# Kernel optimization log

Hardware: AMD Instinct MI355X
Metric: run time of the kernel (lower is better)

## Reference

```python
import jax, jax.numpy as jnp
import numpy as np

EPS = 1e-06
N_HEADS = 32
HEAD_DIM = 128
D_STATE = 128
D_MODEL = 2048
D_INNER = 4096
BATCH = 64


def setup_inputs() -> dict:
    key = jax.random.key(0)
    ks = jax.random.split(key, 8)
    bc_dim = N_HEADS * D_STATE
    theta_dim = N_HEADS * (D_STATE // 2)
    proj_dim = 2 * D_INNER + 2 * bc_dim + 2 * N_HEADS + theta_dim  # 18496
    x = jax.random.normal(ks[0], (BATCH, D_MODEL), jnp.float32)
    h = jax.random.normal(ks[1], (BATCH, N_HEADS, D_STATE, HEAD_DIM), jnp.float32) * 0.1
    B_prev = jax.random.normal(ks[2], (BATCH, N_HEADS, D_STATE), jnp.float32)
    x_prev = jax.random.normal(ks[3], (BATCH, N_HEADS, HEAD_DIM), jnp.float32)
    theta_cumsum = jax.random.normal(ks[4], (BATCH, N_HEADS, D_STATE // 2), jnp.float32)
    W_in = jax.random.normal(ks[5], (proj_dim, D_MODEL), jnp.float32) * 0.02
    # A_log initialized as log(arange(1, d_state+1)) repeated per head
    A_log = jnp.log(jnp.arange(1, D_STATE + 1, dtype=jnp.float32))[None, :].repeat(N_HEADS, axis=0)
    B_bias = jnp.ones((N_HEADS, D_STATE), jnp.float32)
    C_bias = jnp.ones((N_HEADS, D_STATE), jnp.float32)
    W_out = jax.random.normal(ks[6], (D_MODEL, D_INNER), jnp.float32) * 0.02
    return {"x": x, "h": h, "B_prev": B_prev, "x_prev": x_prev,
            "theta_cumsum": theta_cumsum, "W_in": W_in, "A_log": A_log,
            "B_bias": B_bias, "C_bias": C_bias, "W_out": W_out}


def _rms_norm(v):
    # RMS over last dim (v already fp32)
    rms = jnp.sqrt(jnp.mean(v * v, axis=-1, keepdims=True) + EPS)
    return v / rms


def _apply_rope(v, freqs):
    # v: (B,H,N), freqs: (B,H,N//2); interleaved pairs
    vp = v.reshape(*v.shape[:-1], -1, 2)
    c, s = jnp.cos(freqs), jnp.sin(freqs)
    v0, v1 = vp[..., 0], vp[..., 1]
    y0 = v0 * c - v1 * s
    y1 = v0 * s + v1 * c
    return jnp.stack([y0, y1], axis=-1).reshape(v.shape)


def reference(x, h, B_prev, x_prev, theta_cumsum, W_in, A_log, B_bias, C_bias, W_out):
    batch = x.shape[0]
    bc_dim = N_HEADS * D_STATE
    proj = x @ W_in.T  # (B, proj_dim)
    idx = 0
    x_proj = proj[:, idx:idx + D_INNER]; idx += D_INNER
    z = proj[:, idx:idx + D_INNER]; idx += D_INNER
    B_raw = proj[:, idx:idx + bc_dim]; idx += bc_dim
    C_raw = proj[:, idx:idx + bc_dim]; idx += bc_dim
    dt_raw = proj[:, idx:idx + N_HEADS]; idx += N_HEADS
    lam_raw = proj[:, idx:idx + N_HEADS]; idx += N_HEADS
    theta = proj[:, idx:].reshape(batch, N_HEADS, D_STATE // 2)

    x_proj = x_proj.reshape(batch, N_HEADS, HEAD_DIM)
    z = z.reshape(batch, N_HEADS, HEAD_DIM)
    B_raw = B_raw.reshape(batch, N_HEADS, D_STATE)
    C_raw = C_raw.reshape(batch, N_HEADS, D_STATE)

    B = _rms_norm(B_raw) + B_bias
    C = _rms_norm(C_raw) + C_bias

    dt = jax.nn.softplus(dt_raw)                       # (B,H)
    theta_cumsum_new = theta_cumsum + theta * dt[:, :, None]
    B = _apply_rope(B, theta_cumsum_new)
    C = _apply_rope(C, theta_cumsum_new)

    lam = jax.nn.sigmoid(lam_raw)                      # (B,H)
    A = -jnp.mean(jnp.exp(A_log), axis=-1)             # (H,)
    alpha = jnp.exp(dt * A)                            # (B,H)
    beta = (1.0 - lam) * dt * alpha
    gamma = lam * dt

    Bx_prev = jnp.einsum('bhn,bhp->bhnp', B_prev, x_prev)
    Bx_curr = jnp.einsum('bhn,bhp->bhnp', B, x_proj)
    h_new = (alpha[:, :, None, None] * h
             + beta[:, :, None, None] * Bx_prev
             + gamma[:, :, None, None] * Bx_curr)      # (B,H,N,P)

    y = jnp.einsum('bhn,bhnp->bhp', C, h_new)
    y = y * jax.nn.silu(z)
    y = y.reshape(batch, D_INNER) @ W_out.T            # (B, d_model)
    return y, h_new, B, x_proj, theta_cumsum_new
```

## Files before the change

kernel.cpp:

```cpp
#include <hip/hip_runtime.h>
#include <hip/hip_bf16.h>
#include <cstdint>
#include <cmath>

#define EPSV 1e-6f
#define PSTR 1183744

typedef __attribute__((ext_vector_type(8))) short bf16x8;
typedef __attribute__((ext_vector_type(4))) float f32x4;

typedef __attribute__((address_space(3))) unsigned int lds_u32;
typedef const __attribute__((address_space(1))) unsigned int g_u32;

__device__ __forceinline__ void load_lds16(const void* g, void* l) {
  __builtin_amdgcn_global_load_lds((g_u32*)g, (lds_u32*)l, 16, 0, 0);
}

__device__ __forceinline__ short f2b(float f) {
  unsigned u = __float_as_uint(f);
  u = (u + 0x7fffu + ((u >> 16) & 1u)) >> 16;
  return (short)u;
}

__device__ __forceinline__ bf16x8 cvt8(float4 a, float4 b) {
  bf16x8 v;
  v[0]=f2b(a.x); v[1]=f2b(a.y); v[2]=f2b(a.z); v[3]=f2b(a.w);
  v[4]=f2b(b.x); v[5]=f2b(b.y); v[6]=f2b(b.z); v[7]=f2b(b.w);
  return v;
}

__global__ __launch_bounds__(256) void conv_bf16(
    const float* __restrict__ in, short* __restrict__ out, int n8) {
  const int i = blockIdx.x * 256 + threadIdx.x;
  if (i < n8) {
    float4 a = ((const float4*)in)[2 * i];
    float4 b = ((const float4*)in)[2 * i + 1];
    ((bf16x8*)out)[i] = cvt8(a, b);
  }
}

template<int KSPLIT, int NT>
__global__ __launch_bounds__(256, 2) void gemm_wlds(
    const short* __restrict__ Abf, const float* __restrict__ W,
    float* __restrict__ Outp, int N, int K) {
  __shared__ float Wlds[3][64 * 64];
  __shared__ short Alds[3][64 * 64];
  const int tid = threadIdx.x;
  const int lane = tid & 63;
  const int wv = tid >> 6;
  const int lrow = lane & 15, lk = lane >> 4;
  const int bid = blockIdx.x;
  const int ks = bid % KSPLIT;
  const int nblk = (bid / KSPLIT) * 64;
  const int kbase = ks * (NT * 64);

  f32x4 acc[4];
#pragma unroll
  for (int i = 0; i < 4; ++i) acc[i] = (f32x4){0.f, 0.f, 0.f, 0.f};

  auto stage = [&](int buf, int k0) {
#pragma unroll
    for (int j = 0; j < 4; ++j) {
      const int c = wv * 4 + j;
      const int r = c * 4 + (lane >> 4);
      const int g = (lane & 15) ^ (r & 15);
      load_lds16(W + (size_t)(nblk + r) * K + k0 + g * 4,
                 (char*)&Wlds[buf][0] + c * 1024);
    }
#pragma unroll
    for (int j = 0; j < 2; ++j) {
      const int c = wv * 2 + j;
      const int r = c * 8 + (lane >> 3);
      const int g = (lane & 7) ^ (r & 7);
      load_lds16(Abf + (size_t)r * K + k0 + g * 8,
                 (char*)&Alds[buf][0] + c * 1024);
    }
  };

  auto compute = [&](int buf) {
    const int wr = wv * 16 + lrow;
#pragma unroll
    for (int kc = 0; kc < 2; ++kc) {
      const int g0 = kc * 8 + lk * 2;
      const float4 wlo = *(const float4*)((const char*)&Wlds[buf][0]
                          + wr * 256 + ((g0 ^ (lrow & 15)) * 16));
      const float4 whi = *(const float4*)((const char*)&Wlds[buf][0]
                          + wr * 256 + (((g0 + 1) ^ (lrow & 15)) * 16));
      const bf16x8 wb = cvt8(wlo, whi);
#pragma unroll
      for (int mf = 0; mf < 4; ++mf) {
        const int ar = mf * 16 + lrow;
        const int ga = ((kc << 2) | lk) ^ (ar & 7);
        const bf16x8 av = *(const bf16x8*)((const char*)&Alds[buf][0]
                           + ar * 128 + ga * 16);
        acc[mf] = __builtin_amdgcn_mfma_f32_16x16x32_bf16(av, wb, acc[mf], 0, 0, 0);
      }
    }
  };

  stage(0, kbase);
  stage(1, kbase + 64);

  for (int t = 0; t < NT; ++t) {
    if (t < NT - 1) asm volatile("s_waitcnt vmcnt(6)");
    else            asm volatile("s_waitcnt vmcnt(0)");
    __builtin_amdgcn_sched_barrier(0);
    __builtin_amdgcn_s_barrier();
    __builtin_amdgcn_sched_barrier(0);
    compute(t % 3);
    if (t + 2 <= NT - 1) stage((t + 2) % 3, kbase + (t + 2) * 64);
  }

  float* ob = Outp + (size_t)ks * 64 * N + nblk + wv * 16 + lrow;
#pragma unroll
  for (int mf = 0; mf < 4; ++mf)
#pragma unroll
    for (int i = 0; i < 4; ++i)
      ob[(size_t)(mf * 16 + lk * 4 + i) * N] = acc[mf][i];
}

__device__ __forceinline__ float block_reduce_sum256(float v, float* red, int t) {
#pragma unroll
  for (int o = 32; o > 0; o >>= 1) v += __shfl_xor(v, o, 64);
  __syncthreads();
  if ((t & 63) == 0) red[t >> 6] = v;
  __syncthreads();
  return red[0] + red[1] + red[2] + red[3];
}

__global__ __launch_bounds__(256) void state_update(
    const float* __restrict__ pp, const float* __restrict__ h,
    const float* __restrict__ B_prev, const float* __restrict__ x_prev,
    const float* __restrict__ theta_cumsum, const float* __restrict__ A_log,
    const float* __restrict__ B_bias, const float* __restrict__ C_bias,
    float* __restrict__ o_h, float* __restrict__ o_B,
    float* __restrict__ o_xp, float* __restrict__ o_th,
    short* __restrict__ ysbf) {
  const int bid = blockIdx.x;
  const int b = bid >> 5, hd = bid & 31;
  const int t = threadIdx.x;
  const size_t pb = (size_t)b * 18496;
#define PJ(o) (pp[pb + (o)] + pp[PSTR + pb + (o)] + pp[2 * PSTR + pb + (o)] \
             + pp[3 * PSTR + pb + (o)])

  __shared__ float sB[128], sC[128], sBp[128], sXp[128], sXv[128];
  __shared__ float red[8];
  __shared__ float yred[8][128];

  float aval = (t < 128) ? expf(A_log[hd * 128 + t]) : 0.f;
  float brv  = (t < 128) ? PJ(8192 + hd * 128 + t) : 0.f;
  float crv  = (t < 128) ? PJ(12288 + hd * 128 + t) : 0.f;
  if (t < 128) {
    sBp[t] = B_prev[(size_t)bid * 128 + t];
    float xp = PJ(hd * 128 + t);
    sXp[t] = xp;
    o_xp[(size_t)bid * 128 + t] = xp;
    sXv[t] = x_prev[(size_t)bid * 128 + t];
  }
  float sumA  = block_reduce_sum256(aval, red, t);
  float sumB2 = block_reduce_sum256(brv * brv, red, t);
  float sumC2 = block_reduce_sum256(crv * crv, red, t);

  const float dt_raw  = PJ(16384 + hd);
  const float lam_raw = PJ(16416 + hd);
  const float dt  = (dt_raw > 20.f) ? dt_raw : log1pf(expf(dt_raw));
  const float lam = 1.f / (1.f + expf(-lam_raw));
  const float A     = -sumA * (1.f / 128.f);
  const float alpha = expf(dt * A);
  const float beta  = (1.f - lam) * dt * alpha;
  const float gamma = lam * dt;
  const float rb = rsqrtf(sumB2 * (1.f / 128.f) + EPSV);
  const float rc = rsqrtf(sumC2 * (1.f / 128.f) + EPSV);

  if (t < 64) {
    float b0 = PJ(8192 + hd * 128 + 2 * t);
    float b1 = PJ(8192 + hd * 128 + 2 * t + 1);
    float c0 = PJ(12288 + hd * 128 + 2 * t);
    float c1 = PJ(12288 + hd * 128 + 2 * t + 1);
    b0 = b0 * rb + B_bias[hd * 128 + 2 * t];
    b1 = b1 * rb + B_bias[hd * 128 + 2 * t + 1];
    c0 = c0 * rc + C_bias[hd * 128 + 2 * t];
    c1 = c1 * rc + C_bias[hd * 128 + 2 * t + 1];
    const float th = theta_cumsum[(size_t)bid * 64 + t]
                   + PJ(16448 + hd * 64 + t) * dt;
    o_th[(size_t)bid * 64 + t] = th;
    const float cth = cosf(th), sth = sinf(th);
    const float nb0 = b0 * cth - b1 * sth, nb1 = b0 * sth + b1 * cth;
    const float nc0 = c0 * cth - c1 * sth, nc1 = c0 * sth + c1 * cth;
    sB[2 * t] = nb0; sB[2 * t + 1] = nb1;
    sC[2 * t] = nc0; sC[2 * t + 1] = nc1;
    o_B[(size_t)bid * 128 + 2 * t] = nb0;
    o_B[(size_t)bid * 128 + 2 * t + 1] = nb1;
  }
  __syncthreads();

  const int p4 = t & 31, nb = t >> 5;
  const float4 xp4 = *(const float4*)&sXp[p4 * 4];
  const float4 xv4 = *(const float4*)&sXv[p4 * 4];
  const size_t hbase = (size_t)bid * 16384;
  float4 ya = {0.f, 0.f, 0.f, 0.f};
  for (int n = nb; n < 128; n += 8) {
    const float4 hv = *(const float4*)&h[hbase + n * 128 + p4 * 4];
    const float cb = gamma * sB[n];
    const float cp = beta * sBp[n];
    float4 hn;
    hn.x = alpha * hv.x + cp * xv4.x + cb * xp4.x;
    hn.y = alpha * hv.y + cp * xv4.y + cb * xp4.y;
    hn.z = alpha * hv.z + cp * xv4.z + cb * xp4.z;
    hn.w = alpha * hv.w + cp * xv4.w + cb * xp4.w;
    *(float4*)&o_h[hbase + n * 128 + p4 * 4] = hn;
    const float cn = sC[n];
    ya.x += cn * hn.x; ya.y += cn * hn.y; ya.z += cn * hn.z; ya.w += cn * hn.w;
  }
  *(float4*)&yred[nb][p4 * 4] = ya;
  __syncthreads();
  if (t < 128) {
    float y = 0.f;
#pragma unroll
    for (int j = 0; j < 8; ++j) y += yred[j][t];
    const float zv = PJ(4096 + hd * 128 + t);
    const float sig = 1.f / (1.f + expf(-zv));
    ysbf[(size_t)b * 4096 + hd * 128 + t] = f2b(y * zv * sig);
  }
#undef PJ
}

__global__ __launch_bounds__(256) void reduce_y(
    const float* __restrict__ yp, float* __restrict__ y, int n4) {
  const int i = blockIdx.x * 256 + threadIdx.x;
  if (i < n4) {
    float4 s = ((const float4*)yp)[i];
#pragma unroll
    for (int k = 1; k < 16; ++k) {
      float4 t = ((const float4*)(yp + (size_t)k * 131072))[i];
      s.x += t.x; s.y += t.y; s.z += t.z; s.w += t.w;
    }
    ((float4*)y)[i] = s;
  }
}

extern "C" void kernel_launch(void* const* d_in, const int* in_sizes, int n_in,
                              void* d_out, int out_size, void* d_ws, size_t ws_size,
                              hipStream_t stream) {
  const float* x            = (const float*)d_in[0];
  const float* h            = (const float*)d_in[1];
  const float* B_prev       = (const float*)d_in[2];
  const float* x_prev       = (const float*)d_in[3];
  const float* theta_cumsum = (const float*)d_in[4];
  const float* W_in         = (const float*)d_in[5];
  const float* A_log        = (const float*)d_in[6];
  const float* B_bias       = (const float*)d_in[7];
  const float* C_bias       = (const float*)d_in[8];
  const float* W_out        = (const float*)d_in[9];

  float* out  = (float*)d_out;
  float* o_y  = out;
  float* o_h  = out + 131072;
  float* o_B  = o_h + 33554432;
  float* o_xp = o_B + 262144;
  float* o_th = o_xp + 262144;

  float* pp   = (float*)d_ws;
  float* yp   = pp;
  short* xbf  = (short*)(pp + 4 * PSTR);
  short* ysbf = xbf + 131072;

  conv_bf16<<<dim3(64), dim3(256), 0, stream>>>(x, xbf, 16384);
  gemm_wlds<4, 8><<<dim3(289 * 4), dim3(256), 0, stream>>>(
      xbf, W_in, pp, 18496, 2048);
  state_update<<<dim3(2048), dim3(256), 0, stream>>>(
      pp, h, B_prev, x_prev, theta_cumsum, A_log, B_bias, C_bias,
      o_h, o_B, o_xp, o_th, ysbf);
  gemm_wlds<16, 4><<<dim3(32 * 16), dim3(256), 0, stream>>>(
      ysbf, W_out, yp, 2048, 4096);
  reduce_y<<<dim3(128), dim3(256), 0, stream>>>(yp, o_y, 32768);
}
```

Before: 118.2 us.

## Give each wave private LDS tiles and drop block barriers in GEMM

```diff
diff --git a/kernel.cpp b/kernel.cpp
--- a/kernel.cpp
+++ b/kernel.cpp
@@ -40,19 +40,19 @@
 }
 
 template<int KSPLIT, int NT>
-__global__ __launch_bounds__(256, 2) void gemm_wlds(
+__global__ __launch_bounds__(256, 2) void gemm_wave(
     const short* __restrict__ Abf, const float* __restrict__ W,
     float* __restrict__ Outp, int N, int K) {
-  __shared__ float Wlds[3][64 * 64];
-  __shared__ short Alds[3][64 * 64];
-  const int tid = threadIdx.x;
-  const int lane = tid & 63;
-  const int wv = tid >> 6;
+  __shared__ float Wl[4][3][16 * 32];
+  __shared__ short Al[4][3][64 * 32];
+  const int lane = threadIdx.x & 63;
+  const int wv = threadIdx.x >> 6;
   const int lrow = lane & 15, lk = lane >> 4;
   const int bid = blockIdx.x;
   const int ks = bid % KSPLIT;
   const int nblk = (bid / KSPLIT) * 64;
-  const int kbase = ks * (NT * 64);
+  const int n0 = nblk + wv * 16;
+  const int kbase = ks * (NT * 32);
 
   f32x4 acc[4];
 #pragma unroll
@@ -60,58 +60,50 @@
 
   auto stage = [&](int buf, int k0) {
 #pragma unroll
+    for (int j = 0; j < 2; ++j) {
+      const int r = j * 8 + (lane >> 3);
+      const int g = (lane & 7) ^ (r & 7);
+      load_lds16(W + (size_t)(n0 + r) * K + k0 + g * 4,
+                 (char*)&Wl[wv][buf][0] + j * 1024);
+    }
+#pragma unroll
     for (int j = 0; j < 4; ++j) {
-      const int c = wv * 4 + j;
-      const int r = c * 4 + (lane >> 4);
-      const int g = (lane & 15) ^ (r & 15);
-      load_lds16(W + (size_t)(nblk + r) * K + k0 + g * 4,
-                 (char*)&Wlds[buf][0] + c * 1024);
-    }
-#pragma unroll
-    for (int j = 0; j < 2; ++j) {
-      const int c = wv * 2 + j;
-      const int r = c * 8 + (lane >> 3);
-      const int g = (lane & 7) ^ (r & 7);
+      const int r = j * 16 + (lane >> 2);
+      const int g = (lane & 3) ^ ((r >> 1) & 3);
       load_lds16(Abf + (size_t)r * K + k0 + g * 8,
-                 (char*)&Alds[buf][0] + c * 1024);
+                 (char*)&Al[wv][buf][0] + j * 1024);
     }
   };
 
   auto compute = [&](int buf) {
-    const int wr = wv * 16 + lrow;
-#pragma unroll
-    for (int kc = 0; kc < 2; ++kc) {
-      const int g0 = kc * 8 + lk * 2;
-      const float4 wlo = *(const float4*)((const char*)&Wlds[buf][0]
-                          + wr * 256 + ((g0 ^ (lrow & 15)) * 16));
-      const float4 whi = *(const float4*)((const char*)&Wlds[buf][0]
-                          + wr * 256 + (((g0 + 1) ^ (lrow & 15)) * 16));
-      const bf16x8 wb = cvt8(wlo, whi);
-#pragma unroll
-      for (int mf = 0; mf < 4; ++mf) {
-        const int ar = mf * 16 + lrow;
-        const int ga = ((kc << 2) | lk) ^ (ar & 7);
-        const bf16x8 av = *(const bf16x8*)((const char*)&Alds[buf][0]
-                           + ar * 128 + ga * 16);
-        acc[mf] = __builtin_amdgcn_mfma_f32_16x16x32_bf16(av, wb, acc[mf], 0, 0, 0);
-      }
+    const float4 wlo = *(const float4*)((const char*)&Wl[wv][buf][0]
+                        + lrow * 128 + (((2 * lk)     ^ (lrow & 7)) * 16));
+    const float4 whi = *(const float4*)((const char*)&Wl[wv][buf][0]
+                        + lrow * 128 + (((2 * lk + 1) ^ (lrow & 7)) * 16));
+    const bf16x8 wb = cvt8(wlo, whi);
+#pragma unroll
+    for (int mf = 0; mf < 4; ++mf) {
+      const int ar = mf * 16 + lrow;
+      const int ga = lk ^ ((ar >> 1) & 3);
+      const bf16x8 av = *(const bf16x8*)((const char*)&Al[wv][buf][0]
+                         + ar * 64 + ga * 16);
+      acc[mf] = __builtin_amdgcn_mfma_f32_16x16x32_bf16(av, wb, acc[mf], 0, 0, 0);
     }
   };
 
   stage(0, kbase);
-  stage(1, kbase + 64);
+  stage(1, kbase + 32);
 
   for (int t = 0; t < NT; ++t) {
     if (t < NT - 1) asm volatile("s_waitcnt vmcnt(6)");
     else            asm volatile("s_waitcnt vmcnt(0)");
     __builtin_amdgcn_sched_barrier(0);
-    __builtin_amdgcn_s_barrier();
+    if (t + 2 <= NT - 1) stage((t + 2) % 3, kbase + (t + 2) * 32);
     __builtin_amdgcn_sched_barrier(0);
     compute(t % 3);
-    if (t + 2 <= NT - 1) stage((t + 2) % 3, kbase + (t + 2) * 64);
-  }
-
-  float* ob = Outp + (size_t)ks * 64 * N + nblk + wv * 16 + lrow;
+  }
+
+  float* ob = Outp + (size_t)ks * 64 * N + n0 + lrow;
 #pragma unroll
   for (int mf = 0; mf < 4; ++mf)
 #pragma unroll
@@ -266,12 +258,12 @@
   short* ysbf = xbf + 131072;
 
   conv_bf16<<<dim3(64), dim3(256), 0, stream>>>(x, xbf, 16384);
-  gemm_wlds<4, 8><<<dim3(289 * 4), dim3(256), 0, stream>>>(
+  gemm_wave<4, 16><<<dim3(289 * 4), dim3(256), 0, stream>>>(
       xbf, W_in, pp, 18496, 2048);
   state_update<<<dim3(2048), dim3(256), 0, stream>>>(
       pp, h, B_prev, x_prev, theta_cumsum, A_log, B_bias, C_bias,
       o_h, o_B, o_xp, o_th, ysbf);
-  gemm_wlds<16, 4><<<dim3(32 * 16), dim3(256), 0, stream>>>(
+  gemm_wave<16, 8><<<dim3(32 * 16), dim3(256), 0, stream>>>(
       ysbf, W_out, yp, 2048, 4096);
   reduce_y<<<dim3(128), dim3(256), 0, stream>>>(yp, o_y, 32768);
 }
```

After: 128.0 us. +8.2%, slower.

## Use 128-wide N tiles with 32-deep K steps for input projection GEMM

Applied to the files above, without the earlier changes.

```diff
diff --git a/kernel.cpp b/kernel.cpp
--- a/kernel.cpp
+++ b/kernel.cpp
@@ -40,14 +40,98 @@
 }
 
 template<int KSPLIT, int NT>
+__global__ __launch_bounds__(256, 2) void gemm_t128(
+    const short* __restrict__ Abf, const float* __restrict__ W,
+    float* __restrict__ Outp, int N, int K) {
+  __shared__ float Wlds[3][128 * 32];
+  __shared__ short Alds[3][64 * 32];
+  const int lane = threadIdx.x & 63;
+  const int wv = threadIdx.x >> 6;
+  const int lrow = lane & 15, lk = lane >> 4;
+  const int bid = blockIdx.x;
+  const int ks = bid % KSPLIT;
+  const int n0 = (bid / KSPLIT) * 128;
+  const int kbase = ks * (NT * 32);
+
+  f32x4 acc[2][4];
+#pragma unroll
+  for (int a = 0; a < 2; ++a)
+#pragma unroll
+    for (int b = 0; b < 4; ++b) acc[a][b] = (f32x4){0.f, 0.f, 0.f, 0.f};
+
+  auto stage = [&](int buf, int k0) {
+#pragma unroll
+    for (int j = 0; j < 4; ++j) {
+      const int c = wv * 4 + j;
+      const int r = c * 8 + (lane >> 3);
+      const int g = (lane & 7) ^ (r & 7);
+      int gr = n0 + r; if (gr > N - 1) gr = N - 1;
+      load_lds16(W + (size_t)gr * K + k0 + g * 4,
+                 (char*)&Wlds[buf][0] + c * 1024);
+    }
+    {
+      const int r = wv * 16 + (lane >> 2);
+      const int g = (lane & 3) ^ ((r >> 1) & 3);
+      load_lds16(Abf + (size_t)r * K + k0 + g * 8,
+                 (char*)&Alds[buf][0] + wv * 1024);
+    }
+  };
+
+  auto compute = [&](int buf) {
+#pragma unroll
+    for (int mfw = 0; mfw < 2; ++mfw) {
+      const int wr = wv * 32 + mfw * 16 + lrow;
+      const float4 wlo = *(const float4*)((const char*)&Wlds[buf][0]
+                          + wr * 128 + (((2 * lk)     ^ (wr & 7)) * 16));
+      const float4 whi = *(const float4*)((const char*)&Wlds[buf][0]
+                          + wr * 128 + (((2 * lk + 1) ^ (wr & 7)) * 16));
+      const bf16x8 wb = cvt8(wlo, whi);
+#pragma unroll
+      for (int mfa = 0; mfa < 4; ++mfa) {
+        const int ar = mfa * 16 + lrow;
+        const int ga = lk ^ ((ar >> 1) & 3);
+        const bf16x8 av = *(const bf16x8*)((const char*)&Alds[buf][0]
+                           + ar * 64 + ga * 16);
+        acc[mfw][mfa] = __builtin_amdgcn_mfma_f32_16x16x32_bf16(av, wb, acc[mfw][mfa], 0, 0, 0);
+      }
+    }
+  };
+
+  stage(0, kbase);
+  stage(1, kbase + 32);
+
+  for (int t = 0; t < NT; ++t) {
+    if (t < NT - 1) asm volatile("s_waitcnt vmcnt(5)");
+    else            asm volatile("s_waitcnt vmcnt(0)");
+    __builtin_amdgcn_sched_barrier(0);
+    __builtin_amdgcn_s_barrier();
+    __builtin_amdgcn_sched_barrier(0);
+    compute(t % 3);
+    if (t + 2 <= NT - 1) stage((t + 2) % 3, kbase + (t + 2) * 32);
+  }
+
+  float* ob = Outp + (size_t)ks * 64 * N;
+#pragma unroll
+  for (int mfw = 0; mfw < 2; ++mfw) {
+    const int n = n0 + wv * 32 + mfw * 16 + lrow;
+    if (n < N) {
+#pragma unroll
+      for (int mfa = 0; mfa < 4; ++mfa)
+#pragma unroll
+        for (int i = 0; i < 4; ++i)
+          ob[(size_t)(mfa * 16 + lk * 4 + i) * N + n] = acc[mfw][mfa][i];
+    }
+  }
+}
+
+template<int KSPLIT, int NT>
 __global__ __launch_bounds__(256, 2) void gemm_wlds(
     const short* __restrict__ Abf, const float* __restrict__ W,
     float* __restrict__ Outp, int N, int K) {
   __shared__ float Wlds[3][64 * 64];
   __shared__ short Alds[3][64 * 64];
-  const int tid = threadIdx.x;
-  const int lane = tid & 63;
-  const int wv = tid >> 6;
+  const int lane = threadIdx.x & 63;
+  const int wv = threadIdx.x >> 6;
   const int lrow = lane & 15, lk = lane >> 4;
   const int bid = blockIdx.x;
   const int ks = bid % KSPLIT;
@@ -266,7 +350,7 @@
   short* ysbf = xbf + 131072;
 
   conv_bf16<<<dim3(64), dim3(256), 0, stream>>>(x, xbf, 16384);
-  gemm_wlds<4, 8><<<dim3(289 * 4), dim3(256), 0, stream>>>(
+  gemm_t128<4, 16><<<dim3(145 * 4), dim3(256), 0, stream>>>(
       xbf, W_in, pp, 18496, 2048);
   state_update<<<dim3(2048), dim3(256), 0, stream>>>(
       pp, h, B_prev, x_prev, theta_cumsum, A_log, B_bias, C_bias,
```

After: 126.9 us. +7.4%, slower.
